# Kernel tuning notes

Measured on AMD Instinct MI355X. Metric: run time of the kernel, lower is better.

The kernel has to match this reference:

```python
import jax, jax.numpy as jnp
import numpy as np
import math

B = 2
H = 16
M = 1024
D = 64      # head_dim
P = 1024    # persistent memory size
SPAN = 1024 # external attention span


def setup_inputs() -> dict:
    key = jax.random.key(0)
    k1, k2, k3, k4 = jax.random.split(key, 4)
    query = jax.random.normal(k1, (B * H, M, D), dtype=jnp.float32)
    attn = jax.random.normal(k2, (B * H, M, SPAN), dtype=jnp.float32)
    # params as in __init__
    pkey = jax.random.normal(k3, (H, D, P), dtype=jnp.float32) / math.sqrt(D)
    pval = jax.random.normal(k4, (H, P, D), dtype=jnp.float32) / math.sqrt(P)
    return {"query": query, "attn": attn, "key": pkey, "val": pval}


def reference(query, attn, key, val):
    h, d, p = key.shape
    bh, m, _ = query.shape
    q = query.reshape(-1, h, m, d)                      # [B,H,M,D]
    # attn_pers = q @ (key * sqrt(d)); later divided by sqrt(d) -> net q@key
    attn_pers = jnp.einsum('bhmd,hdp->bhmp', q, key * math.sqrt(d))
    attn_pers = attn_pers.reshape(-1, m, p)             # [B*H,M,P]
    scores = jnp.concatenate([attn, attn_pers], axis=-1) / math.sqrt(d)
    probs = jax.nn.softmax(scores, axis=-1)             # [B*H,M,SPAN+P]
    attn_out = probs[:, :, :-p]                         # [B*H,M,SPAN]
    pers = probs[:, :, -p:].reshape(-1, h, m, p)        # [B,H,M,P]
    out = jnp.einsum('bhmp,hpd->bhmd', pers, val * math.sqrt(p))
    out = out.reshape(-1, m, d)                         # [B*H,M,D]
    return (attn_out, out)
```

## Files before the change

kernel.cpp:

```cpp
#include <hip/hip_runtime.h>
#include <hip/hip_bf16.h>
#include <math.h>

#define BH   32
#define NH   16
#define MM   1024
#define DD   64
#define PP   1024
#define SPAN 1024

typedef unsigned short ushort_t;
typedef __attribute__((ext_vector_type(8))) short  short8;
typedef __attribute__((ext_vector_type(4))) float  f32x4;

#define MFMA(a,b,c) __builtin_amdgcn_mfma_f32_16x16x32_bf16(a,b,c,0,0,0)

#if __has_builtin(__builtin_amdgcn_exp2f)
#define EXP2(x) __builtin_amdgcn_exp2f(x)
#else
#define EXP2(x) __expf((x) * 0.6931471805599453f)
#endif

#define ATTN_SC 0.18033688011111603f
#define LOG2E   1.4426950408889634f

#define WS_SP0_OFF (4194304ull)
#define WS_SP1_OFF (4325376ull)
#define WS_O1_OFF  (4456448ull)
#define WS_NEED    (12845056ull)

__device__ __forceinline__ ushort_t f2bf(float x) {
    __hip_bfloat16 b = __float2bfloat16(x);
    return __builtin_bit_cast(unsigned short, b);
}
__device__ __forceinline__ float bf2f(ushort_t u) {
    __hip_bfloat16 b = __builtin_bit_cast(__hip_bfloat16, u);
    return __bfloat162float(b);
}

__launch_bounds__(256)
__global__ void pm_pre(const float* __restrict__ key,
                       const float* __restrict__ val,
                       ushort_t* __restrict__ wsKV)
{
    int bi = blockIdx.x, t = threadIdx.x;
    if (bi < 512) {
        int id = bi * 256 + t;
        int l  = id & 63;
        int ks = (id >> 6) & 1;
        int pb = (id >> 7) & 3;
        int c  = (id >> 9) & 15;
        int h  = (id >> 13) & 15;
        int p     = c * 64 + pb * 16 + (l & 15);
        int dbase = ks * 32 + (l >> 4) * 8;
        size_t fo = (size_t)(h * 16 + c) * 8192 + (size_t)(pb * 2 + ks) * 512 + (size_t)l * 8;
#pragma unroll
        for (int e = 0; e < 8; ++e)
            wsKV[fo + e] = f2bf(key[(size_t)(h * 64 + dbase + e) * PP + p] * LOG2E);
    } else {
        int id = (bi - 512) * 256 + t;
        int l   = id & 63;
        int db  = (id >> 6) & 3;
        int ks2 = (id >> 8) & 1;
        int c   = (id >> 9) & 15;
        int h   = (id >> 13) & 15;
        int d = db * 16 + (l & 15);
        size_t fo = (size_t)(h * 16 + c) * 8192 + 4096 + (size_t)(ks2 * 4 + db) * 512 + (size_t)l * 8;
#pragma unroll
        for (int e = 0; e < 8; ++e) {
            int p = c * 64 + ks2 * 32 + ((l >> 4) * 4) + (e & 3) + 16 * (e >> 2);
            wsKV[fo + e] = f2bf(val[(size_t)(h * PP + p) * DD + d]);
        }
    }
}

__launch_bounds__(256)
__global__ void pm_flash(const float* __restrict__ q,
                         const ushort_t* __restrict__ wsKV,
                         float* __restrict__ ws_sp0,
                         float* __restrict__ ws_sp1,
                         float* __restrict__ o1,
                         float* __restrict__ out)
{
    __shared__ ushort_t kvbuf[2][8192];

    const int t  = threadIdx.x;
    const int w  = t >> 6;
    const int l  = t & 63;
    const int bi = blockIdx.x;
    const int hi = l >> 4;
    const int lo = l & 15;

    const int s    = bi & 1;
    const int unit = bi >> 1;
    const int bh   = unit & 31;
    const int tile = unit >> 5;
    const int h    = bh & (NH - 1);
    const size_t rowbase = (size_t)bh * MM + tile * 64;

    short8 qf[2][2];
    {
        const float* qr = q + (rowbase + w * 16 + lo) * DD + hi * 8;
#pragma unroll
        for (int ks = 0; ks < 2; ++ks) {
            float4 a = *(const float4*)(qr + ks * 32);
            float4 b = *(const float4*)(qr + ks * 32 + 4);
            float f[8] = {a.x, a.y, a.z, a.w, b.x, b.y, b.z, b.w};
            short8 qh, ql;
#pragma unroll
            for (int e = 0; e < 8; ++e) {
                ushort_t hh = f2bf(f[e]);
                qh[e] = (short)hh;
                ql[e] = (short)f2bf(f[e] - bf2f(hh));
            }
            qf[ks][0] = qh;
            qf[ks][1] = ql;
        }
    }

    const ushort_t* KVb = wsKV + (size_t)h * (16 * 8192);

    auto STAGE = [&](int b, int c) {
        const char* src = (const char*)(KVb + (size_t)c * 8192) + w * 4096 + l * 16;
        char* dst = (char*)&kvbuf[b][0] + w * 4096;
#pragma unroll
        for (int j = 0; j < 4; ++j)
            __builtin_amdgcn_global_load_lds(
                (const __attribute__((address_space(1))) void*)(src + j * 1024),
                (__attribute__((address_space(3))) void*)(dst + j * 1024),
                16, 0, 0);
    };

    f32x4 oacc[4] = {{0.f,0.f,0.f,0.f},{0.f,0.f,0.f,0.f},{0.f,0.f,0.f,0.f},{0.f,0.f,0.f,0.f}};
    float spart = 0.f;

    STAGE(0, s * 8);
    __syncthreads();

    for (int cc = 0; cc < 8; ++cc) {
        const int cur = cc & 1;
        if (cc < 7) STAGE(cur ^ 1, s * 8 + cc + 1);

        const ushort_t* Kc = &kvbuf[cur][0];
        const ushort_t* Vc = Kc + 4096;

        f32x4 sacc[4] = {{0.f,0.f,0.f,0.f},{0.f,0.f,0.f,0.f},{0.f,0.f,0.f,0.f},{0.f,0.f,0.f,0.f}};
        __builtin_amdgcn_s_setprio(1);
#pragma unroll
        for (int pb = 0; pb < 4; ++pb) {
#pragma unroll
            for (int ks = 0; ks < 2; ++ks) {
                short8 khi = *(const short8*)(Kc + (pb * 2 + ks) * 512 + l * 8);
                sacc[pb] = MFMA(khi, qf[ks][0], sacc[pb]);
                sacc[pb] = MFMA(khi, qf[ks][1], sacc[pb]);
            }
        }
        __builtin_amdgcn_s_setprio(0);

        float ep[4][4];
#pragma unroll
        for (int pb = 0; pb < 4; ++pb)
#pragma unroll
            for (int r = 0; r < 4; ++r) {
                float pv = EXP2(sacc[pb][r]);
                ep[pb][r] = pv;
                spart += pv;
            }

        short8 pf[2][2];
#pragma unroll
        for (int ks2 = 0; ks2 < 2; ++ks2) {
            short8 phi8, plo8;
#pragma unroll
            for (int e = 0; e < 8; ++e) {
                float pv = ep[ks2 * 2 + (e >> 2)][e & 3];
                ushort_t hh = f2bf(pv);
                phi8[e] = (short)hh;
                plo8[e] = (short)f2bf(pv - bf2f(hh));
            }
            pf[ks2][0] = phi8;
            pf[ks2][1] = plo8;
        }

        __builtin_amdgcn_s_setprio(1);
#pragma unroll
        for (int ks2 = 0; ks2 < 2; ++ks2) {
#pragma unroll
            for (int db = 0; db < 4; ++db) {
                short8 vhi = *(const short8*)(Vc + (ks2 * 4 + db) * 512 + l * 8);
                oacc[db] = MFMA(pf[ks2][0], vhi, oacc[db]);
                oacc[db] = MFMA(pf[ks2][1], vhi, oacc[db]);
            }
        }
        __builtin_amdgcn_s_setprio(0);

        __syncthreads();
    }

    spart += __shfl_xor(spart, 16);
    spart += __shfl_xor(spart, 32);
    float* spdst = s ? ws_sp1 : ws_sp0;
    if (hi == 0) spdst[rowbase + w * 16 + lo] = spart;

    float* odst = s ? o1 : out;
#pragma unroll
    for (int reg = 0; reg < 4; ++reg) {
        const size_t ro = (rowbase + w * 16 + hi * 4 + reg) * DD + lo;
#pragma unroll
        for (int db = 0; db < 4; ++db)
            __builtin_nontemporal_store(oacc[db][reg], &odst[ro + db * 16]);
    }
}

__launch_bounds__(256)
__global__ void pm_norm(const float* __restrict__ attn,
                        const float* __restrict__ ws_sp0,
                        const float* __restrict__ ws_sp1,
                        const float* __restrict__ o1,
                        float* __restrict__ attn_out,
                        float* __restrict__ out)
{
    const int t = threadIdx.x;
    const int w = t >> 6;
    const int l = t & 63;
    const size_t row = (size_t)blockIdx.x * 4 + w;

    const f32x4* arow = (const f32x4*)(attn + row * SPAN);
    f32x4 av[4];
#pragma unroll
    for (int j = 0; j < 4; ++j) av[j] = arow[j * 64 + l];

    float sm = 0.f;
#pragma unroll
    for (int j = 0; j < 4; ++j)
#pragma unroll
        for (int e = 0; e < 4; ++e) {
            av[j][e] = EXP2(av[j][e] * ATTN_SC);
            sm += av[j][e];
        }
#pragma unroll
    for (int s = 1; s < 64; s <<= 1) sm += __shfl_xor(sm, s);

    const float iZ = 1.f / (sm + ws_sp0[row] + ws_sp1[row]);

    f32x4* orow = (f32x4*)(attn_out + row * SPAN);
#pragma unroll
    for (int j = 0; j < 4; ++j)
        __builtin_nontemporal_store(av[j] * iZ, orow + j * 64 + l);

    const float ov0 = out[row * DD + l];
    const float ov1 = o1[row * DD + l];
    __builtin_nontemporal_store((ov0 + ov1) * 32.f * iZ, &out[row * DD + l]);
}

__launch_bounds__(256)
__global__ void pm_fallback(const float* __restrict__ q,
                            const float* __restrict__ attn,
                            const float* __restrict__ key,
                            const float* __restrict__ val,
                            float* __restrict__ attn_out,
                            float* __restrict__ out)
{
    __shared__ float qs[64][68];
    __shared__ float ks[64][68];
    __shared__ float vs[64][DD];
    __shared__ float sc[64][66];
    __shared__ float rmax[64];
    __shared__ float rsum[64];

    const int t    = threadIdx.x;
    const int bh   = blockIdx.y;
    const int tile = blockIdx.x;
    const int h    = bh & (NH - 1);
    const int m0   = tile * 64;
    const int tr   = t >> 4;
    const int tc   = t & 15;
    const int r0   = tr * 4;
    const int c0   = tc * 4;
    const int lane = t & 63;
    const int wave = t >> 6;

    const size_t qbase = (size_t)bh * MM * DD + (size_t)m0 * DD;
    const size_t abase = (size_t)bh * MM * SPAN + (size_t)m0 * SPAN;
    const size_t kbase = (size_t)h * DD * PP;
    const size_t vbase = (size_t)h * PP * DD;

#pragma unroll
    for (int j = 0; j < 16; ++j) {
        int idx = j * 256 + t;
        int r = idx >> 6, d = idx & 63;
        qs[r][d] = q[qbase + (size_t)r * DD + d];
    }
    for (int rr = 0; rr < 16; ++rr) {
        int r = wave * 16 + rr;
        const float* arow = attn + abase + (size_t)r * SPAN;
        float av[16];
        float mx = -INFINITY;
#pragma unroll
        for (int j = 0; j < 16; ++j) { av[j] = arow[j * 64 + lane] * 0.125f; mx = fmaxf(mx, av[j]); }
#pragma unroll
        for (int s = 32; s; s >>= 1) mx = fmaxf(mx, __shfl_xor(mx, s));
        float sm = 0.f;
#pragma unroll
        for (int j = 0; j < 16; ++j) sm += __expf(av[j] - mx);
#pragma unroll
        for (int s = 32; s; s >>= 1) sm += __shfl_xor(sm, s);
        if (lane == 0) { rmax[r] = mx; rsum[r] = sm; }
    }
    __syncthreads();
    for (int p0 = 0; p0 < PP; p0 += 64) {
        if (p0) __syncthreads();
#pragma unroll
        for (int j = 0; j < 16; ++j) {
            int idx = j * 256 + t;
            int d = idx >> 6, pc = idx & 63;
            ks[pc][d] = key[kbase + (size_t)d * PP + p0 + pc];
        }
        __syncthreads();
        float acc[4][4] = {};
#pragma unroll
        for (int d0 = 0; d0 < DD; d0 += 4) {
            float4 q4[4], k4[4];
#pragma unroll
            for (int rr = 0; rr < 4; ++rr) q4[rr] = *(const float4*)&qs[r0 + rr][d0];
#pragma unroll
            for (int cc = 0; cc < 4; ++cc) k4[cc] = *(const float4*)&ks[c0 + cc][d0];
#pragma unroll
            for (int rr = 0; rr < 4; ++rr)
#pragma unroll
                for (int cc = 0; cc < 4; ++cc)
                    acc[rr][cc] += q4[rr].x * k4[cc].x + q4[rr].y * k4[cc].y
                                 + q4[rr].z * k4[cc].z + q4[rr].w * k4[cc].w;
        }
#pragma unroll
        for (int rr = 0; rr < 4; ++rr) {
            float mx = fmaxf(fmaxf(acc[rr][0], acc[rr][1]), fmaxf(acc[rr][2], acc[rr][3]));
#pragma unroll
            for (int s = 8; s; s >>= 1) mx = fmaxf(mx, __shfl_xor(mx, s));
            float sm = 0.f;
#pragma unroll
            for (int cc = 0; cc < 4; ++cc) sm += __expf(acc[rr][cc] - mx);
#pragma unroll
            for (int s = 8; s; s >>= 1) sm += __shfl_xor(sm, s);
            if (tc == 0) {
                int r = r0 + rr;
                float om = rmax[r], os = rsum[r];
                float nm = fmaxf(om, mx);
                rsum[r] = os * __expf(om - nm) + sm * __expf(mx - nm);
                rmax[r] = nm;
            }
        }
    }
    __syncthreads();
    for (int rr = 0; rr < 16; ++rr) {
        int r = wave * 16 + rr;
        float Mx = rmax[r];
        float iZv = 1.0f / rsum[r];
        const float* arow = attn + abase + (size_t)r * SPAN;
        float* orow = attn_out + abase + (size_t)r * SPAN;
#pragma unroll
        for (int j = 0; j < 16; ++j) {
            float a = arow[j * 64 + lane] * 0.125f;
            orow[j * 64 + lane] = __expf(a - Mx) * iZv;
        }
    }
    float acc2[4][4] = {};
    for (int p0 = 0; p0 < PP; p0 += 64) {
        __syncthreads();
#pragma unroll
        for (int j = 0; j < 16; ++j) {
            int idx = j * 256 + t;
            int d = idx >> 6, pc = idx & 63;
            ks[pc][d] = key[kbase + (size_t)d * PP + p0 + pc];
        }
#pragma unroll
        for (int j = 0; j < 16; ++j) {
            int idx = j * 256 + t;
            int pc = idx >> 6, d = idx & 63;
            vs[pc][d] = val[vbase + (size_t)(p0 + pc) * DD + d];
        }
        __syncthreads();
        float acc[4][4] = {};
#pragma unroll
        for (int d0 = 0; d0 < DD; d0 += 4) {
            float4 q4[4], k4[4];
#pragma unroll
            for (int rr = 0; rr < 4; ++rr) q4[rr] = *(const float4*)&qs[r0 + rr][d0];
#pragma unroll
            for (int cc = 0; cc < 4; ++cc) k4[cc] = *(const float4*)&ks[c0 + cc][d0];
#pragma unroll
            for (int rr = 0; rr < 4; ++rr)
#pragma unroll
                for (int cc = 0; cc < 4; ++cc)
                    acc[rr][cc] += q4[rr].x * k4[cc].x + q4[rr].y * k4[cc].y
                                 + q4[rr].z * k4[cc].z + q4[rr].w * k4[cc].w;
        }
#pragma unroll
        for (int rr = 0; rr < 4; ++rr) {
            float Mx = rmax[r0 + rr];
#pragma unroll
            for (int cc = 0; cc < 4; ++cc)
                sc[r0 + rr][c0 + cc] = __expf(acc[rr][cc] - Mx);
        }
        __syncthreads();
        for (int pc = 0; pc < 64; ++pc) {
            float4 v4 = *(const float4*)&vs[pc][tc * 4];
#pragma unroll
            for (int rr = 0; rr < 4; ++rr) {
                float pr = sc[r0 + rr][pc];
                acc2[rr][0] += pr * v4.x;
                acc2[rr][1] += pr * v4.y;
                acc2[rr][2] += pr * v4.z;
                acc2[rr][3] += pr * v4.w;
            }
        }
    }
#pragma unroll
    for (int rr = 0; rr < 4; ++rr) {
        int r = r0 + rr;
        float s = 32.0f / rsum[r];
        float4 o;
        o.x = acc2[rr][0] * s; o.y = acc2[rr][1] * s;
        o.z = acc2[rr][2] * s; o.w = acc2[rr][3] * s;
        *(float4*)&out[(size_t)bh * MM * DD + (size_t)(m0 + r) * DD + tc * 4] = o;
    }
}

extern "C" void kernel_launch(void* const* d_in, const int* in_sizes, int n_in,
                              void* d_out, int out_size, void* d_ws, size_t ws_size,
                              hipStream_t stream) {
    const float* q    = (const float*)d_in[0];
    const float* attn = (const float*)d_in[1];
    const float* key  = (const float*)d_in[2];
    const float* val  = (const float*)d_in[3];
    float* attn_out = (float*)d_out;
    float* out      = (float*)d_out + (size_t)BH * MM * SPAN;

    if (ws_size >= WS_NEED) {
        ushort_t* wsKV   = (ushort_t*)d_ws;
        float*    ws_sp0 = (float*)((char*)d_ws + WS_SP0_OFF);
        float*    ws_sp1 = (float*)((char*)d_ws + WS_SP1_OFF);
        float*    o1     = (float*)((char*)d_ws + WS_O1_OFF);
        pm_pre  <<<1024, 256, 0, stream>>>(key, val, wsKV);
        pm_flash<<<1024, 256, 0, stream>>>(q, wsKV, ws_sp0, ws_sp1, o1, out);
        pm_norm <<<8192, 256, 0, stream>>>(attn, ws_sp0, ws_sp1, o1, attn_out, out);
    } else {
        dim3 grid(MM / 64, BH);
        pm_fallback<<<grid, 256, 0, stream>>>(q, attn, key, val, attn_out, out);
    }
}
```

Baseline: 75.54 us.

## Precompute attn row exp-sums in the pre kernel so the norm kernel streams once

```diff
diff --git a/kernel.cpp b/kernel.cpp
--- a/kernel.cpp
+++ b/kernel.cpp
@@ -26,8 +26,9 @@
 
 #define WS_SP0_OFF (4194304ull)
 #define WS_SP1_OFF (4325376ull)
-#define WS_O1_OFF  (4456448ull)
-#define WS_NEED    (12845056ull)
+#define WS_SA_OFF  (4456448ull)
+#define WS_O1_OFF  (4587520ull)
+#define WS_NEED    (12976128ull)
 
 __device__ __forceinline__ ushort_t f2bf(float x) {
     __hip_bfloat16 b = __float2bfloat16(x);
@@ -39,9 +40,11 @@
 }
 
 __launch_bounds__(256)
-__global__ void pm_pre(const float* __restrict__ key,
-                       const float* __restrict__ val,
-                       ushort_t* __restrict__ wsKV)
+__global__ void pm_pre_stats(const float* __restrict__ key,
+                             const float* __restrict__ val,
+                             const float* __restrict__ attn,
+                             ushort_t* __restrict__ wsKV,
+                             float* __restrict__ ws_sa)
 {
     int bi = blockIdx.x, t = threadIdx.x;
     if (bi < 512) {
@@ -57,7 +60,7 @@
 #pragma unroll
         for (int e = 0; e < 8; ++e)
             wsKV[fo + e] = f2bf(key[(size_t)(h * 64 + dbase + e) * PP + p] * LOG2E);
-    } else {
+    } else if (bi < 1024) {
         int id = (bi - 512) * 256 + t;
         int l   = id & 63;
         int db  = (id >> 6) & 3;
@@ -70,6 +73,25 @@
         for (int e = 0; e < 8; ++e) {
             int p = c * 64 + ks2 * 32 + ((l >> 4) * 4) + (e & 3) + 16 * (e >> 2);
             wsKV[fo + e] = f2bf(val[(size_t)(h * PP + p) * DD + d]);
+        }
+    } else {
+        const int w = t >> 6;
+        const int l = t & 63;
+        const size_t rbase = ((size_t)(bi - 1024) * 16) + (size_t)w * 4;
+        for (int rr = 0; rr < 4; ++rr) {
+            const size_t row = rbase + rr;
+            const f32x4* arow = (const f32x4*)(attn + row * SPAN);
+            f32x4 av[4];
+#pragma unroll
+            for (int j = 0; j < 4; ++j) av[j] = arow[j * 64 + l];
+            float sm = 0.f;
+#pragma unroll
+            for (int j = 0; j < 4; ++j)
+#pragma unroll
+                for (int e = 0; e < 4; ++e) sm += EXP2(av[j][e] * ATTN_SC);
+#pragma unroll
+            for (int s = 1; s < 64; s <<= 1) sm += __shfl_xor(sm, s);
+            if (l == 0) ws_sa[row] = sm;
         }
     }
 }
@@ -213,44 +235,34 @@
 }
 
 __launch_bounds__(256)
-__global__ void pm_norm(const float* __restrict__ attn,
-                        const float* __restrict__ ws_sp0,
-                        const float* __restrict__ ws_sp1,
-                        const float* __restrict__ o1,
-                        float* __restrict__ attn_out,
-                        float* __restrict__ out)
+__global__ void pm_scale(const float* __restrict__ attn,
+                         const float* __restrict__ ws_sa,
+                         const float* __restrict__ ws_sp0,
+                         const float* __restrict__ ws_sp1,
+                         const float* __restrict__ o1,
+                         float* __restrict__ attn_out,
+                         float* __restrict__ out)
 {
     const int t = threadIdx.x;
     const int w = t >> 6;
     const int l = t & 63;
     const size_t row = (size_t)blockIdx.x * 4 + w;
 
+    const float iZ = 1.f / (ws_sa[row] + ws_sp0[row] + ws_sp1[row]);
+
     const f32x4* arow = (const f32x4*)(attn + row * SPAN);
-    f32x4 av[4];
-#pragma unroll
-    for (int j = 0; j < 4; ++j) av[j] = arow[j * 64 + l];
-
-    float sm = 0.f;
-#pragma unroll
-    for (int j = 0; j < 4; ++j)
-#pragma unroll
-        for (int e = 0; e < 4; ++e) {
-            av[j][e] = EXP2(av[j][e] * ATTN_SC);
-            sm += av[j][e];
-        }
-#pragma unroll
-    for (int s = 1; s < 64; s <<= 1) sm += __shfl_xor(sm, s);
-
-    const float iZ = 1.f / (sm + ws_sp0[row] + ws_sp1[row]);
-
-    f32x4* orow = (f32x4*)(attn_out + row * SPAN);
-#pragma unroll
-    for (int j = 0; j < 4; ++j)
-        __builtin_nontemporal_store(av[j] * iZ, orow + j * 64 + l);
-
-    const float ov0 = out[row * DD + l];
-    const float ov1 = o1[row * DD + l];
-    __builtin_nontemporal_store((ov0 + ov1) * 32.f * iZ, &out[row * DD + l]);
+    f32x4*       orow = (f32x4*)(attn_out + row * SPAN);
+#pragma unroll
+    for (int j = 0; j < 4; ++j) {
+        f32x4 a = arow[j * 64 + l];
+        f32x4 o;
+#pragma unroll
+        for (int e = 0; e < 4; ++e) o[e] = EXP2(a[e] * ATTN_SC) * iZ;
+        __builtin_nontemporal_store(o, orow + j * 64 + l);
+    }
+
+    const float ov = out[row * DD + l] + o1[row * DD + l];
+    __builtin_nontemporal_store(ov * 32.f * iZ, &out[row * DD + l]);
 }
 
 __launch_bounds__(256)
@@ -440,10 +452,11 @@
         ushort_t* wsKV   = (ushort_t*)d_ws;
         float*    ws_sp0 = (float*)((char*)d_ws + WS_SP0_OFF);
         float*    ws_sp1 = (float*)((char*)d_ws + WS_SP1_OFF);
+        float*    ws_sa  = (float*)((char*)d_ws + WS_SA_OFF);
         float*    o1     = (float*)((char*)d_ws + WS_O1_OFF);
-        pm_pre  <<<1024, 256, 0, stream>>>(key, val, wsKV);
-        pm_flash<<<1024, 256, 0, stream>>>(q, wsKV, ws_sp0, ws_sp1, o1, out);
-        pm_norm <<<8192, 256, 0, stream>>>(attn, ws_sp0, ws_sp1, o1, attn_out, out);
+        pm_pre_stats<<<3072, 256, 0, stream>>>(key, val, attn, wsKV, ws_sa);
+        pm_flash    <<<1024, 256, 0, stream>>>(q, wsKV, ws_sp0, ws_sp1, o1, out);
+        pm_scale    <<<8192, 256, 0, stream>>>(attn, ws_sa, ws_sp0, ws_sp1, o1, attn_out, out);
     } else {
         dim3 grid(MM / 64, BH);
         pm_fallback<<<grid, 256, 0, stream>>>(q, attn, key, val, attn_out, out);
```

After: 91.93 us. 21.7% more time.
